# Optimization experiments

Hardware: AMD Instinct MI355X
Metric: run time of the kernel (lower is better)

Reference implementation:

```python
import jax, jax.numpy as jnp
import numpy as np

B, T, N, D, F = 4, 64, 128, 256, 512
LN_EPS = 1e-5


def _ln(x, g, b):
    m = jnp.mean(x, -1, keepdims=True)
    v = jnp.var(x, -1, keepdims=True)
    return (x - m) * jax.lax.rsqrt(v + LN_EPS) * g + b


def _norm_adj(cirmat):
    # dense_to_sparse drops edge weights -> binary adjacency; gcn_norm adds
    # remaining self loops (diag forced to weight 1) and sym-normalizes.
    a = (cirmat != 0).astype(jnp.float32)
    a = jnp.where(jnp.eye(a.shape[0], dtype=bool), 1.0, a)
    deg = a.sum(0)  # aggregation at col index -> in-degree
    dinv = jax.lax.rsqrt(deg)
    return a * dinv[:, None] * dinv[None, :]


def _block_mpnn(x, a_hat, ng, nb, w1, b1, sg, sb, gw, gb, w2, b2):
    # x: [B,T,N,D]. gMLP block whose spatial proj is a GCNConv over the N axis.
    res = x
    h = jax.nn.gelu(_ln(x, ng, nb) @ w1.T + b1, approximate=False)  # [B,T,N,2F]
    u, v = jnp.split(h, 2, axis=-1)
    vn = _ln(v, sg, sb)
    # GCNConv: lin -> normalized aggregation (edge r->c, sum at c) -> +bias
    g = jnp.einsum('rc,btrf->btcf', a_hat, vn @ gw.T) + gb
    return (u * g) @ w2.T + b2 + res


def _block_conv(x, ng, nb, w1, b1, sg, sb, cw, cb, w2, b2):
    # x: [B,N,T,D]. Conv2d(T, T, kernel=(1,3), padding=(0,1)) mixes the T axis
    # as channels with a width-3 window along the feature axis.
    res = x
    h = jax.nn.gelu(_ln(x, ng, nb) @ w1.T + b1, approximate=False)  # [B,N,T,2F]
    u, v = jnp.split(h, 2, axis=-1)
    vn = _ln(v, sg, sb).transpose(0, 2, 1, 3)  # [B,T,N,F] = NCHW
    c = jax.lax.conv_general_dilated(
        vn, cw, window_strides=(1, 1), padding=((0, 0), (1, 1)),
        dimension_numbers=('NCHW', 'OIHW', 'NCHW'))
    g = (c + cb[None, :, None, None]).transpose(0, 2, 1, 3)  # [B,N,T,F]
    return (u * g) @ w2.T + b2 + res


def setup_inputs():
    key = jax.random.key(0)
    cnt = [0]
    def nk():
        cnt[0] += 1
        return jax.random.fold_in(key, cnt[0])
    def rn(shape, s=1.0):
        return jax.random.normal(nk(), shape, jnp.float32) * s
    inp = {}
    inp['x'] = rn((B, T, N, D))
    inp['cirmat'] = jax.random.randint(nk(), (N, N), 0, 2, jnp.int32)
    for p in ('tgu', 'sgu', 'cgu'):
        inp[p + '_ng'] = jnp.ones((D,), jnp.float32)
        inp[p + '_nb'] = jnp.zeros((D,), jnp.float32)
        inp[p + '_w1'] = rn((2 * F, D), 0.02)
        inp[p + '_b1'] = jnp.zeros((2 * F,), jnp.float32)
        inp[p + '_sg'] = jnp.ones((F,), jnp.float32)
        inp[p + '_sb'] = jnp.zeros((F,), jnp.float32)
        inp[p + '_w2'] = rn((D, F), 0.02)
        inp[p + '_b2'] = jnp.zeros((D,), jnp.float32)
    inp['tgu_cw'] = rn((T, T, 1, 3), 0.02)
    inp['tgu_cb'] = jnp.ones((T,), jnp.float32)  # nn.init.constant_(bias, 1.0)
    inp['sgu_gw'] = rn((F, F), 0.02)
    inp['sgu_gb'] = jnp.ones((F,), jnp.float32)
    inp['cgu_gw'] = rn((F, F), 0.02)
    inp['cgu_gb'] = jnp.ones((F,), jnp.float32)
    for n in ('n1', 'n2', 'n3'):
        inp[n + '_g'] = jnp.ones((D,), jnp.float32)
        inp[n + '_b'] = jnp.zeros((D,), jnp.float32)
    inp['w_out'] = rn((D, 3 * D), 0.02)
    inp['b_out'] = jnp.zeros((D,), jnp.float32)
    return inp


def reference(x, cirmat,
              tgu_ng, tgu_nb, tgu_w1, tgu_b1, tgu_sg, tgu_sb, tgu_w2, tgu_b2,
              sgu_ng, sgu_nb, sgu_w1, sgu_b1, sgu_sg, sgu_sb, sgu_w2, sgu_b2,
              cgu_ng, cgu_nb, cgu_w1, cgu_b1, cgu_sg, cgu_sb, cgu_w2, cgu_b2,
              tgu_cw, tgu_cb, sgu_gw, sgu_gb, cgu_gw, cgu_gb,
              n1_g, n1_b, n2_g, n2_b, n3_g, n3_b, w_out, b_out):
    a_hat = _norm_adj(cirmat)
    res = x
    # temporal branch: permute to [B,N,T,D], conv mixer, permute back
    xt = _block_conv(x.transpose(0, 2, 1, 3), tgu_ng, tgu_nb, tgu_w1, tgu_b1,
                     tgu_sg, tgu_sb, tgu_cw, tgu_cb, tgu_w2, tgu_b2)
    xt = _ln(xt.transpose(0, 2, 1, 3), n1_g, n1_b)
    # spatial (GCN) branch; note: the block shadows the passed residual with x
    xs = _ln(_block_mpnn(x, a_hat, sgu_ng, sgu_nb, sgu_w1, sgu_b1, sgu_sg,
                         sgu_sb, sgu_gw, sgu_gb, sgu_w2, sgu_b2), n2_g, n2_b)
    # cycle (GCN) branch (pe=None -> another mpnn block on cirmat_A)
    xc = _ln(_block_mpnn(x, a_hat, cgu_ng, cgu_nb, cgu_w1, cgu_b1, cgu_sg,
                         cgu_sb, cgu_gw, cgu_gb, cgu_w2, cgu_b2), n3_g, n3_b)
    cat = jnp.concatenate([xt, xs, xc], axis=-1)  # [B,T,N,3D]
    # 1x1 Conv2d over the channel (last) dim == linear projection
    return cat @ w_out.T + b_out + res
```

## Files before the change

### kernel.cpp

```cpp
#include <hip/hip_runtime.h>
#include <hip/hip_bf16.h>

typedef unsigned short u16;
typedef unsigned int u32;
typedef __attribute__((ext_vector_type(4))) float f32x4;
typedef __attribute__((ext_vector_type(8))) short short8;

#define DEV __device__ __forceinline__

constexpr int Bc = 4, Tc = 64, Nc = 128, Dc = 256, Fc = 512;
constexpr int R = Bc * Tc * Nc;

constexpr size_t OFF_ABIN = 0;
constexpr size_t OFF_DINV = 65536;
constexpr size_t OFF_COLS = 66560;
constexpr size_t OFF_AHT  = 67584;
constexpr size_t OFF_W1   = 100352;
constexpr size_t OFF_B1   = 1673216;
constexpr size_t OFF_GW   = 1685504;
constexpr size_t OFF_CVEC = 2734080;
constexpr size_t OFF_W2   = 2738176;
constexpr size_t OFF_BW   = 3524608;
constexpr size_t OFF_BTOT = 3917824;
constexpr size_t OFF_CWT  = 3918848;
constexpr size_t OFF_XHAT = 4194304;
constexpr size_t OFF_U    = 20971520;
constexpr size_t OFF_V    = 54525952;
constexpr size_t OFF_S3   = 88080384;
constexpr size_t OFF_Y    = 121634816;
constexpr size_t WS_NEED  = 171966464;

DEV u16 f2b(float f) { __hip_bfloat16 h = __float2bfloat16(f); return *(u16*)&h; }
DEV float b2f(u16 u) { union { u32 i; float f; } v; v.i = ((u32)u) << 16; return v.f; }
DEV u32 pack2(float a, float b) { return (u32)f2b(a) | ((u32)f2b(b) << 16); }
DEV float wave_sum(float s) {
  #pragma unroll
  for (int o = 32; o; o >>= 1) s += __shfl_xor(s, o);
  return s;
}
DEV float gelu(float v) {
  float t = v * v;
  float e = __expf(v * (1.5957691f + 0.0713548162f * t));
  return v - v * __builtin_amdgcn_rcpf(e + 1.0f);
}
DEV void gload16(const u16* g, u16* l) {
  __builtin_amdgcn_global_load_lds((const __attribute__((address_space(1))) void*)g,
                                   (__attribute__((address_space(3))) void*)l, 16, 0, 0);
}
DEV void wait_vm0()   { asm volatile("s_waitcnt vmcnt(0)" ::: "memory");  __builtin_amdgcn_sched_barrier(0); }
DEV void wait_lgkm0() { asm volatile("s_waitcnt lgkmcnt(0)" ::: "memory"); __builtin_amdgcn_sched_barrier(0); }

__global__ void k_adj1(const int* __restrict__ cir, float* __restrict__ aBin) {
  int r = blockIdx.x, c = threadIdx.x;
  aBin[r * 128 + c] = (cir[r * 128 + c] != 0 || r == c) ? 1.f : 0.f;
}
__global__ void k_adj2(const float* __restrict__ aBin, float* __restrict__ dinv) {
  int c = threadIdx.x; float s = 0.f;
  for (int r = 0; r < 128; r++) s += aBin[r * 128 + c];
  dinv[c] = rsqrtf(s);
}
__global__ void k_adj3(const float* __restrict__ aBin, const float* __restrict__ dinv,
                       u16* __restrict__ ahatT) {
  int c = blockIdx.x, r = threadIdx.x;
  ahatT[c * 128 + r] = f2b(aBin[r * 128 + c] * dinv[r] * dinv[c]);
}
__global__ void k_adj4(const float* __restrict__ aBin, const float* __restrict__ dinv,
                       float* __restrict__ colsum) {
  int c = threadIdx.x; float s = 0.f;
  for (int r = 0; r < 128; r++) s += aBin[r * 128 + c] * dinv[r];
  colsum[c] = s * dinv[c];
}

__global__ void k_prep_w1(const float* __restrict__ w1, const float* __restrict__ ng,
                          const float* __restrict__ nb, const float* __restrict__ b1,
                          u16* __restrict__ w1o, float* __restrict__ b1o) {
  int k = blockIdx.x, lane = threadIdx.x;
  float4 wv = *(const float4*)(w1 + k * 256 + lane * 4);
  float4 gv = *(const float4*)(ng + lane * 4);
  float4 bv = *(const float4*)(nb + lane * 4);
  uint2 o; o.x = pack2(wv.x * gv.x, wv.y * gv.y); o.y = pack2(wv.z * gv.z, wv.w * gv.w);
  *(uint2*)(w1o + k * 256 + lane * 4) = o;
  float acc = wv.x * bv.x + wv.y * bv.y + wv.z * bv.z + wv.w * bv.w;
  acc = wave_sum(acc);
  if (lane == 0) b1o[k] = b1[k] + acc;
}
__global__ void k_prep_gw(const float* __restrict__ gw, const float* __restrict__ sg,
                          const float* __restrict__ sb, u16* __restrict__ gwo,
                          float* __restrict__ cvo) {
  int f = blockIdx.x, lane = threadIdx.x;
  float acc = 0.f; uint4 o;
  float4 w0 = *(const float4*)(gw + f * 512 + lane * 8);
  float4 w1 = *(const float4*)(gw + f * 512 + lane * 8 + 4);
  float4 g0 = *(const float4*)(sg + lane * 8);
  float4 g1 = *(const float4*)(sg + lane * 8 + 4);
  float4 b0 = *(const float4*)(sb + lane * 8);
  float4 b1 = *(const float4*)(sb + lane * 8 + 4);
  o.x = pack2(w0.x * g0.x, w0.y * g0.y); o.y = pack2(w0.z * g0.z, w0.w * g0.w);
  o.z = pack2(w1.x * g1.x, w1.y * g1.y); o.w = pack2(w1.z * g1.z, w1.w * g1.w);
  acc = w0.x * b0.x + w0.y * b0.y + w0.z * b0.z + w0.w * b0.w
      + w1.x * b1.x + w1.y * b1.y + w1.z * b1.z + w1.w * b1.w;
  *(uint4*)(gwo + f * 512 + lane * 8) = o;
  acc = wave_sum(acc);
  if (lane == 0) cvo[f] = acc;
}
__global__ void k_b16cvt(const float* __restrict__ src, u16* __restrict__ dst) {
  int idx = (blockIdx.x * 64 + threadIdx.x) * 8;
  float4 a = *(const float4*)(src + idx);
  float4 b = *(const float4*)(src + idx + 4);
  uint4 o; o.x = pack2(a.x, a.y); o.y = pack2(a.z, a.w);
  o.z = pack2(b.x, b.y); o.w = pack2(b.z, b.w);
  *(uint4*)(dst + idx) = o;
}
__global__ void k_prep_wout(const float* __restrict__ wout, const float* __restrict__ bout,
                            const float* __restrict__ g1, const float* __restrict__ b1,
                            const float* __restrict__ g2, const float* __restrict__ b2,
                            const float* __restrict__ g3, const float* __restrict__ b3,
                            u16* __restrict__ bw, float* __restrict__ bt) {
  int o = blockIdx.x, lane = threadIdx.x;
  float acc = 0.f;
  #pragma unroll
  for (int j = 0; j < 12; j++) {
    int c = lane + j * 64;
    int p = c >> 8, i = c & 255;
    const float* gg = (p == 0) ? g1 : (p == 1) ? g2 : g3;
    const float* bb = (p == 0) ? b1 : (p == 1) ? b2 : b3;
    float w = wout[o * 768 + c];
    bw[o * 768 + c] = f2b(w * gg[i]);
    acc += w * bb[i];
  }
  acc = wave_sum(acc);
  if (lane == 0) bt[o] = bout[o] + acc;
}
__global__ void k_prep_cwA(const float* __restrict__ cw, u16* __restrict__ cwA) {
  int t = blockIdx.x, q = threadIdx.x;
  int tap = q >> 6, ti = q & 63;
  cwA[t * 192 + q] = f2b(cw[t * 192 + ti * 3 + tap]);
}

__global__ __launch_bounds__(256) void k_ln1(const float* __restrict__ x, u16* __restrict__ xhat) {
  int row = blockIdx.x * 4 + (threadIdx.x >> 6);
  int lane = threadIdx.x & 63;
  float4 v = *(const float4*)(x + (size_t)row * 256 + lane * 4);
  float s = v.x + v.y + v.z + v.w;
  float s2 = v.x * v.x + v.y * v.y + v.z * v.z + v.w * v.w;
  s = wave_sum(s); s2 = wave_sum(s2);
  float m = s * (1.f / 256.f);
  float var = s2 * (1.f / 256.f) - m * m;
  float rs = rsqrtf(var + 1e-5f);
  uint2 o; o.x = pack2((v.x - m) * rs, (v.y - m) * rs); o.y = pack2((v.z - m) * rs, (v.w - m) * rs);
  *(uint2*)(xhat + (size_t)row * 256 + lane * 4) = o;
}

template <int MODE>
__global__ __launch_bounds__(256) void k_lnv(const u16* __restrict__ Vin, u16* __restrict__ Vout,
                                             const float* __restrict__ sg, const float* __restrict__ sb) {
  int row = blockIdx.x * 4 + (threadIdx.x >> 6);
  int lane = threadIdx.x & 63;
  uint4 raw = *(const uint4*)(Vin + (size_t)row * 512 + lane * 8);
  u16* rp = (u16*)&raw;
  float f[8], s = 0.f, s2 = 0.f;
  #pragma unroll
  for (int j = 0; j < 8; j++) { f[j] = b2f(rp[j]); s += f[j]; s2 += f[j] * f[j]; }
  s = wave_sum(s); s2 = wave_sum(s2);
  float m = s * (1.f / 512.f);
  float var = s2 * (1.f / 512.f) - m * m;
  float rs = rsqrtf(var + 1e-5f);
  float o[8];
  if (MODE == 1) {
    float4 g0 = *(const float4*)(sg + lane * 8);
    float4 g1 = *(const float4*)(sg + lane * 8 + 4);
    float4 b0 = *(const float4*)(sb + lane * 8);
    float4 b1 = *(const float4*)(sb + lane * 8 + 4);
    o[0] = (f[0] - m) * rs * g0.x + b0.x; o[1] = (f[1] - m) * rs * g0.y + b0.y;
    o[2] = (f[2] - m) * rs * g0.z + b0.z; o[3] = (f[3] - m) * rs * g0.w + b0.w;
    o[4] = (f[4] - m) * rs * g1.x + b1.x; o[5] = (f[5] - m) * rs * g1.y + b1.y;
    o[6] = (f[6] - m) * rs * g1.z + b1.z; o[7] = (f[7] - m) * rs * g1.w + b1.w;
  } else {
    #pragma unroll
    for (int j = 0; j < 8; j++) o[j] = (f[j] - m) * rs;
  }
  uint4 ov; ov.x = pack2(o[0], o[1]); ov.y = pack2(o[2], o[3]);
  ov.z = pack2(o[4], o[5]); ov.w = pack2(o[6], o[7]);
  *(uint4*)(Vout + (size_t)row * 512 + lane * 8) = ov;
}

__global__ __launch_bounds__(256) void k_lny(const float* __restrict__ Y, u16* __restrict__ Ycat, int colofs) {
  int row = blockIdx.x * 4 + (threadIdx.x >> 6);
  int lane = threadIdx.x & 63;
  float4 v = *(const float4*)(Y + (size_t)row * 256 + lane * 4);
  float s = v.x + v.y + v.z + v.w;
  float s2 = v.x * v.x + v.y * v.y + v.z * v.z + v.w * v.w;
  s = wave_sum(s); s2 = wave_sum(s2);
  float m = s * (1.f / 256.f);
  float var = s2 * (1.f / 256.f) - m * m;
  float rs = rsqrtf(var + 1e-5f);
  uint2 o; o.x = pack2((v.x - m) * rs, (v.y - m) * rs); o.y = pack2((v.z - m) * rs, (v.w - m) * rs);
  *(uint2*)(Ycat + (size_t)row * 768 + colofs + lane * 4) = o;
}

template <int KDIM>
DEV void stage_tile(const u16* __restrict__ G, u16* lds, int row0, int tid) {
  #pragma unroll
  for (int i = 0; i < 4; i++) {
    int qq = tid + i * 256;
    int row = qq >> 3, kc = qq & 7;
    int kg = kc ^ (row & 7);
    gload16(G + (size_t)(row0 + row) * KDIM + kg * 8, lds + qq * 8);
  }
}

DEV void mfma_step(const u16* As, const u16* Bs, f32x4 (&acc)[4][4], int lane, int wr, int wc) {
  #pragma unroll
  for (int kk = 0; kk < 2; kk++) {
    int kb = kk * 64 + (lane >> 4) * 16;
    short8 af[4], bfr[4];
    #pragma unroll
    for (int m = 0; m < 4; m++) {
      int row = wr * 64 + m * 16 + (lane & 15);
      af[m] = *(const short8*)((const char*)As + ((row * 128 + kb) ^ ((row & 7) << 4)));
    }
    #pragma unroll
    for (int n = 0; n < 4; n++) {
      int col = wc * 64 + n * 16 + (lane & 15);
      bfr[n] = *(const short8*)((const char*)Bs + ((col * 128 + kb) ^ ((col & 7) << 4)));
    }
    #pragma unroll
    for (int m = 0; m < 4; m++)
      #pragma unroll
      for (int n = 0; n < 4; n++)
        acc[m][n] = __builtin_amdgcn_mfma_f32_16x16x32_bf16(af[m], bfr[n], acc[m][n], 0, 0, 0);
  }
}

template <int KDIM, int EPI>
__global__ __launch_bounds__(256) void k_gemm(const u16* __restrict__ A, const u16* __restrict__ Bt,
                                              const float* __restrict__ bias,
                                              const float* __restrict__ xres,
                                              void* __restrict__ out0, void* __restrict__ out1) {
  __shared__ __align__(16) u16 lds[4 * 8192];
  u16* As[2] = { lds, lds + 16384 };
  u16* Bs[2] = { lds + 8192, lds + 24576 };
  const int tid = threadIdx.x;
  const int lane = tid & 63, wid = tid >> 6;
  const int wr = wid >> 1, wc = wid & 1;
  const int rowA0 = blockIdx.x * 128;
  const int colB0 = blockIdx.y * 128;
  constexpr int NT = KDIM / 64;

  f32x4 zero = {0.f, 0.f, 0.f, 0.f};
  f32x4 acc[4][4];
  #pragma unroll
  for (int m = 0; m < 4; m++)
    #pragma unroll
    for (int n = 0; n < 4; n++) acc[m][n] = zero;

  stage_tile<KDIM>(A, As[0], rowA0, tid);
  stage_tile<KDIM>(Bt, Bs[0], colB0, tid);
  wait_vm0();
  __builtin_amdgcn_s_barrier();

  #pragma unroll
  for (int it = 0; it < NT; ++it) {
    const int cur = it & 1;
    if (it + 1 < NT) {
      stage_tile<KDIM>(A + (it + 1) * 64, As[cur ^ 1], rowA0, tid);
      stage_tile<KDIM>(Bt + (it + 1) * 64, Bs[cur ^ 1], colB0, tid);
    }
    mfma_step(As[cur], Bs[cur], acc, lane, wr, wc);
    wait_lgkm0();
    wait_vm0();
    __builtin_amdgcn_s_barrier();
  }

  #pragma unroll
  for (int m = 0; m < 4; m++) {
    #pragma unroll
    for (int n = 0; n < 4; n++) {
      int col = colB0 + wc * 64 + n * 16 + (lane & 15);
      #pragma unroll
      for (int r = 0; r < 4; r++) {
        int row = rowA0 + wr * 64 + m * 16 + (lane >> 4) * 4 + r;
        float v = acc[m][n][r];
        if (EPI == 0) {
          v = gelu(v + bias[col]);
          u16 hv = f2b(v);
          if (col < 512) ((u16*)out0)[(size_t)row * 512 + col] = hv;
          else           ((u16*)out1)[(size_t)row * 512 + col - 512] = hv;
        } else {
          v += bias[col] + xres[(size_t)row * 256 + col];
          ((float*)out0)[(size_t)row * 256 + col] = v;
        }
      }
    }
  }
}

__global__ __launch_bounds__(256) void k_gcn(const u16* __restrict__ A, const u16* __restrict__ Bt,
                                             const u16* __restrict__ U, const u16* __restrict__ ahatT,
                                             const float* __restrict__ colsum, const float* __restrict__ cvec,
                                             const float* __restrict__ gb, u16* __restrict__ ug) {
  __shared__ __align__(16) char smem[65536];
  u16* As[2] = { (u16*)smem, (u16*)(smem + 32768) };
  u16* Bs[2] = { (u16*)(smem + 16384), (u16*)(smem + 49152) };
  u16* glinT = (u16*)smem;
  const int tid = threadIdx.x;
  const int lane = tid & 63, wid = tid >> 6;
  const int wr = wid >> 1, wc = wid & 1;
  const int bt = blockIdx.x;
  const int rowA0 = bt * 128;
  const int colB0 = blockIdx.y * 128;

  f32x4 zero = {0.f, 0.f, 0.f, 0.f};
  f32x4 acc[4][4];
  #pragma unroll
  for (int m = 0; m < 4; m++)
    #pragma unroll
    for (int n = 0; n < 4; n++) acc[m][n] = zero;

  stage_tile<512>(A, As[0], rowA0, tid);
  stage_tile<512>(Bt, Bs[0], colB0, tid);
  wait_vm0();
  __builtin_amdgcn_s_barrier();
  #pragma unroll
  for (int it = 0; it < 8; ++it) {
    const int cur = it & 1;
    if (it + 1 < 8) {
      stage_tile<512>(A + (it + 1) * 64, As[cur ^ 1], rowA0, tid);
      stage_tile<512>(Bt + (it + 1) * 64, Bs[cur ^ 1], colB0, tid);
    }
    mfma_step(As[cur], Bs[cur], acc, lane, wr, wc);
    wait_lgkm0();
    wait_vm0();
    __builtin_amdgcn_s_barrier();
  }

  #pragma unroll
  for (int m = 0; m < 4; m++) {
    #pragma unroll
    for (int n = 0; n < 4; n++) {
      int f = wc * 64 + n * 16 + (lane & 15);
      int n0 = wr * 64 + m * 16 + (lane >> 4) * 4;
      u32* p = (u32*)(glinT + f * 136 + n0);
      p[0] = pack2(acc[m][n][0], acc[m][n][1]);
      p[1] = pack2(acc[m][n][2], acc[m][n][3]);
    }
  }
  __syncthreads();

  f32x4 acc2[4][4];
  #pragma unroll
  for (int m = 0; m < 4; m++)
    #pragma unroll
    for (int n = 0; n < 4; n++) acc2[m][n] = zero;
  #pragma unroll
  for (int ks = 0; ks < 4; ks++) {
    short8 a2[4], b2v[4];
    #pragma unroll
    for (int m = 0; m < 4; m++) {
      int c = wr * 64 + m * 16 + (lane & 15);
      a2[m] = *(const short8*)(ahatT + c * 128 + ks * 32 + (lane >> 4) * 8);
    }
    #pragma unroll
    for (int n = 0; n < 4; n++) {
      int f = wc * 64 + n * 16 + (lane & 15);
      b2v[n] = *(const short8*)(glinT + f * 136 + ks * 32 + (lane >> 4) * 8);
    }
    #pragma unroll
    for (int m = 0; m < 4; m++)
      #pragma unroll
      for (int n = 0; n < 4; n++)
        acc2[m][n] = __builtin_amdgcn_mfma_f32_16x16x32_bf16(a2[m], b2v[n], acc2[m][n], 0, 0, 0);
  }

  #pragma unroll
  for (int m = 0; m < 4; m++) {
    #pragma unroll
    for (int n = 0; n < 4; n++) {
      int fl = wc * 64 + n * 16 + (lane & 15);
      int fg = colB0 + fl;
      float cv = cvec[fg], gbv = gb[fg];
      #pragma unroll
      for (int r = 0; r < 4; r++) {
        int c = wr * 64 + m * 16 + (lane >> 4) * 4 + r;
        size_t row = (size_t)(rowA0 + c) * 512 + fg;
        float g = b2f(U[row]) * (acc2[m][n][r] + colsum[c] * cv + gbv);
        ug[row] = f2b(g);
      }
    }
  }
}

__global__ __launch_bounds__(256) void k_convm(const u16* __restrict__ vn, const u16* __restrict__ U,
                                               const u16* __restrict__ cwA, const float* __restrict__ cb,
                                               u16* __restrict__ ug) {
  __shared__ __align__(16) u16 vnT[258 * 72];
  int bx = blockIdx.x;
  int n = bx & 127, b = (bx >> 7) & 3, h = bx >> 9;
  int tid = threadIdx.x;
  int lane = tid & 63, wid = tid >> 6;

  {
    int ti = tid & 63;
    size_t rowbase = ((size_t)((b * 64 + ti) * 128 + n)) * 512;
    #pragma unroll
    for (int it = 0; it < 8; it++) {
      int fq = (tid >> 6) + it * 4;
      uint4 raw = *(const uint4*)(vn + rowbase + h * 256 + fq * 8);
      u16* rp = (u16*)&raw;
      int vr = fq * 8 + 1;
      #pragma unroll
      for (int j = 0; j < 8; j++) vnT[(vr + j) * 72 + ti] = rp[j];
    }
    if (tid < 64) {
      vnT[0 * 72 + ti]   = (h == 0) ? (u16)0 : vn[rowbase + 255];
      vnT[257 * 72 + ti] = (h == 1) ? (u16)0 : vn[rowbase + 256];
    }
  }
  __syncthreads();

  f32x4 zero = {0.f, 0.f, 0.f, 0.f};
  f32x4 acc[4][4];
  #pragma unroll
  for (int m = 0; m < 4; m++)
    #pragma unroll
    for (int nn = 0; nn < 4; nn++) acc[m][nn] = zero;

  #pragma unroll
  for (int s = 0; s < 6; s++) {
    int tap = s >> 1;
    int K0 = s * 32;
    int tig = (s & 1) * 32 + (lane >> 4) * 8;
    short8 af[4], bf[4];
    #pragma unroll
    for (int m = 0; m < 4; m++) {
      int t = m * 16 + (lane & 15);
      af[m] = *(const short8*)(cwA + t * 192 + K0 + (lane >> 4) * 8);
    }
    #pragma unroll
    for (int nn = 0; nn < 4; nn++) {
      int fl = wid * 64 + nn * 16 + (lane & 15);
      int vr = fl + tap;
      bf[nn] = *(const short8*)(vnT + vr * 72 + tig);
    }
    #pragma unroll
    for (int m = 0; m < 4; m++)
      #pragma unroll
      for (int nn = 0; nn < 4; nn++)
        acc[m][nn] = __builtin_amdgcn_mfma_f32_16x16x32_bf16(af[m], bf[nn], acc[m][nn], 0, 0, 0);
  }

  #pragma unroll
  for (int m = 0; m < 4; m++) {
    #pragma unroll
    for (int nn = 0; nn < 4; nn++) {
      int fl = wid * 64 + nn * 16 + (lane & 15);
      int fg = h * 256 + fl;
      #pragma unroll
      for (int r = 0; r < 4; r++) {
        int t = m * 16 + (lane >> 4) * 4 + r;
        size_t row = ((size_t)((b * 64 + t) * 128 + n)) * 512 + fg;
        float g = b2f(U[row]) * (acc[m][nn][r] + cb[t]);
        ug[row] = f2b(g);
      }
    }
  }
}

extern "C" void kernel_launch(void* const* d_in, const int* in_sizes, int n_in,
                              void* d_out, int out_size, void* d_ws, size_t ws_size,
                              hipStream_t stream) {
  if (ws_size < WS_NEED) return;
  const float* x = (const float*)d_in[0];
  const int* cir = (const int*)d_in[1];
  auto F32 = [&](int i) { return (const float*)d_in[i]; };

  char* W = (char*)d_ws;
  float* aBin   = (float*)(W + OFF_ABIN);
  float* dinv   = (float*)(W + OFF_DINV);
  float* colsum = (float*)(W + OFF_COLS);
  u16*   ahatT  = (u16*)(W + OFF_AHT);
  u16*   W1c    = (u16*)(W + OFF_W1);
  float* b1c    = (float*)(W + OFF_B1);
  u16*   GWc    = (u16*)(W + OFF_GW);
  float* cvec   = (float*)(W + OFF_CVEC);
  u16*   W2c    = (u16*)(W + OFF_W2);
  u16*   BW     = (u16*)(W + OFF_BW);
  float* btot   = (float*)(W + OFF_BTOT);
  u16*   cwA    = (u16*)(W + OFF_CWT);
  u16*   xhat   = (u16*)(W + OFF_XHAT);
  u16*   Ub     = (u16*)(W + OFF_U);
  u16*   Vb     = (u16*)(W + OFF_V);
  u16*   S3     = (u16*)(W + OFF_S3);
  u16*   Ycat   = (u16*)(W + OFF_Y);

  k_adj1<<<128, 128, 0, stream>>>(cir, aBin);
  k_adj2<<<1, 128, 0, stream>>>(aBin, dinv);
  k_adj3<<<128, 128, 0, stream>>>(aBin, dinv, ahatT);
  k_adj4<<<1, 128, 0, stream>>>(aBin, dinv, colsum);
  for (int p = 0; p < 3; p++) {
    int base = 2 + 8 * p;
    k_prep_w1<<<1024, 64, 0, stream>>>(F32(base + 2), F32(base + 0), F32(base + 1), F32(base + 3),
                                       W1c + (size_t)p * 1024 * 256, b1c + p * 1024);
    k_b16cvt<<<256, 64, 0, stream>>>(F32(base + 6), W2c + (size_t)p * 256 * 512);
  }
  k_prep_gw<<<512, 64, 0, stream>>>(F32(28), F32(14), F32(15), GWc, cvec);
  k_prep_gw<<<512, 64, 0, stream>>>(F32(30), F32(22), F32(23), GWc + 512 * 512, cvec + 512);
  k_prep_wout<<<256, 64, 0, stream>>>(F32(38), F32(39), F32(32), F32(33), F32(34), F32(35),
                                      F32(36), F32(37), BW, btot);
  k_prep_cwA<<<64, 192, 0, stream>>>(F32(26), cwA);

  k_ln1<<<8192, 256, 0, stream>>>(x, xhat);

  k_gemm<256, 0><<<dim3(256, 8), 256, 0, stream>>>(xhat, W1c, b1c, nullptr, Ub, Vb);
  k_lnv<1><<<8192, 256, 0, stream>>>(Vb, S3, F32(6), F32(7));
  k_convm<<<1024, 256, 0, stream>>>(S3, Ub, cwA, F32(27), Vb);
  k_gemm<512, 2><<<dim3(256, 2), 256, 0, stream>>>(Vb, W2c, F32(9), x, (void*)S3, nullptr);
  k_lny<<<8192, 256, 0, stream>>>((const float*)S3, Ycat, 0);

  k_gemm<256, 0><<<dim3(256, 8), 256, 0, stream>>>(xhat, W1c + (size_t)1 * 1024 * 256, b1c + 1024,
                                                   nullptr, Ub, Vb);
  k_lnv<0><<<8192, 256, 0, stream>>>(Vb, S3, nullptr, nullptr);
  k_gcn<<<dim3(256, 4), 256, 0, stream>>>(S3, GWc, Ub, ahatT, colsum, cvec, F32(29), Vb);
  k_gemm<512, 2><<<dim3(256, 2), 256, 0, stream>>>(Vb, W2c + (size_t)1 * 256 * 512, F32(17), x,
                                                   (void*)S3, nullptr);
  k_lny<<<8192, 256, 0, stream>>>((const float*)S3, Ycat, 256);

  k_gemm<256, 0><<<dim3(256, 8), 256, 0, stream>>>(xhat, W1c + (size_t)2 * 1024 * 256, b1c + 2048,
                                                   nullptr, Ub, Vb);
  k_lnv<0><<<8192, 256, 0, stream>>>(Vb, S3, nullptr, nullptr);
  k_gcn<<<dim3(256, 4), 256, 0, stream>>>(S3, GWc + 512 * 512, Ub, ahatT, colsum, cvec + 512, F32(31), Vb);
  k_gemm<512, 2><<<dim3(256, 2), 256, 0, stream>>>(Vb, W2c + (size_t)2 * 256 * 512, F32(25), x,
                                                   (void*)S3, nullptr);
  k_lny<<<8192, 256, 0, stream>>>((const float*)S3, Ycat, 512);

  k_gemm<768, 2><<<dim3(256, 2), 256, 0, stream>>>(Ycat, BW, btot, x, d_out, nullptr);
}
```

Before: 595.0 us.

## Fold GCN-branch LayerNorm into GEMM epilogues and deepen k-loop prefetch

The W1 GEMM epilogue now accumulates per-row sum and sum-of-squares of the v half via shuffles and atomics. The GCN kernel then applies the LayerNorm algebraically on its output, using rs*acc - rs*mean*rowsum(gw*sg). This removes the separate k_lnv pass and its full read/write of V for the two GCN branches. The GEMM k-loop also moves to a two-stage prefetch with vmcnt(8) partial waits, and the adjacency precompute skips the intermediate float matrix. In exchange it adds atomics, memsets and a one-pass variance computation that is less numerically robust.

```diff
diff --git a/kernel.cpp b/kernel.cpp
--- a/kernel.cpp
+++ b/kernel.cpp
@@ -11,18 +11,19 @@
 constexpr int Bc = 4, Tc = 64, Nc = 128, Dc = 256, Fc = 512;
 constexpr int R = Bc * Tc * Nc;
 
-constexpr size_t OFF_ABIN = 0;
-constexpr size_t OFF_DINV = 65536;
-constexpr size_t OFF_COLS = 66560;
-constexpr size_t OFF_AHT  = 67584;
-constexpr size_t OFF_W1   = 100352;
-constexpr size_t OFF_B1   = 1673216;
-constexpr size_t OFF_GW   = 1685504;
-constexpr size_t OFF_CVEC = 2734080;
-constexpr size_t OFF_W2   = 2738176;
-constexpr size_t OFF_BW   = 3524608;
-constexpr size_t OFF_BTOT = 3917824;
-constexpr size_t OFF_CWT  = 3918848;
+constexpr size_t OFF_DINV = 0;
+constexpr size_t OFF_COLS = 1024;
+constexpr size_t OFF_AHT  = 2048;
+constexpr size_t OFF_W1   = 34816;
+constexpr size_t OFF_B1   = 1607680;
+constexpr size_t OFF_GW   = 1619968;
+constexpr size_t OFF_CVEC = 2668544;
+constexpr size_t OFF_GWS  = 2672640;
+constexpr size_t OFF_W2   = 2676736;
+constexpr size_t OFF_BW   = 3463168;
+constexpr size_t OFF_BTOT = 3856384;
+constexpr size_t OFF_CWA  = 3857408;
+constexpr size_t OFF_VST  = 3881984;
 constexpr size_t OFF_XHAT = 4194304;
 constexpr size_t OFF_U    = 20971520;
 constexpr size_t OFF_V    = 54525952;
@@ -47,27 +48,27 @@
   __builtin_amdgcn_global_load_lds((const __attribute__((address_space(1))) void*)g,
                                    (__attribute__((address_space(3))) void*)l, 16, 0, 0);
 }
+DEV void wait_lgkm0() { asm volatile("s_waitcnt lgkmcnt(0)" ::: "memory"); __builtin_amdgcn_sched_barrier(0); }
 DEV void wait_vm0()   { asm volatile("s_waitcnt vmcnt(0)" ::: "memory");  __builtin_amdgcn_sched_barrier(0); }
-DEV void wait_lgkm0() { asm volatile("s_waitcnt lgkmcnt(0)" ::: "memory"); __builtin_amdgcn_sched_barrier(0); }
-
-__global__ void k_adj1(const int* __restrict__ cir, float* __restrict__ aBin) {
-  int r = blockIdx.x, c = threadIdx.x;
-  aBin[r * 128 + c] = (cir[r * 128 + c] != 0 || r == c) ? 1.f : 0.f;
-}
-__global__ void k_adj2(const float* __restrict__ aBin, float* __restrict__ dinv) {
+DEV void wait_vm8()   { asm volatile("s_waitcnt vmcnt(8)" ::: "memory");  __builtin_amdgcn_sched_barrier(0); }
+
+DEV float adj(const int* cir, int r, int c) {
+  return (cir[r * 128 + c] != 0 || r == c) ? 1.f : 0.f;
+}
+__global__ void k_adj2(const int* __restrict__ cir, float* __restrict__ dinv) {
   int c = threadIdx.x; float s = 0.f;
-  for (int r = 0; r < 128; r++) s += aBin[r * 128 + c];
+  for (int r = 0; r < 128; r++) s += adj(cir, r, c);
   dinv[c] = rsqrtf(s);
 }
-__global__ void k_adj3(const float* __restrict__ aBin, const float* __restrict__ dinv,
+__global__ void k_adj3(const int* __restrict__ cir, const float* __restrict__ dinv,
                        u16* __restrict__ ahatT) {
   int c = blockIdx.x, r = threadIdx.x;
-  ahatT[c * 128 + r] = f2b(aBin[r * 128 + c] * dinv[r] * dinv[c]);
-}
-__global__ void k_adj4(const float* __restrict__ aBin, const float* __restrict__ dinv,
+  ahatT[c * 128 + r] = f2b(adj(cir, r, c) * dinv[r] * dinv[c]);
+}
+__global__ void k_adj4(const int* __restrict__ cir, const float* __restrict__ dinv,
                        float* __restrict__ colsum) {
   int c = threadIdx.x; float s = 0.f;
-  for (int r = 0; r < 128; r++) s += aBin[r * 128 + c] * dinv[r];
+  for (int r = 0; r < 128; r++) s += adj(cir, r, c) * dinv[r];
   colsum[c] = s * dinv[c];
 }
 
@@ -86,22 +87,25 @@
 }
 __global__ void k_prep_gw(const float* __restrict__ gw, const float* __restrict__ sg,
                           const float* __restrict__ sb, u16* __restrict__ gwo,
-                          float* __restrict__ cvo) {
+                          float* __restrict__ cvo, float* __restrict__ gwso) {
   int f = blockIdx.x, lane = threadIdx.x;
-  float acc = 0.f; uint4 o;
+  uint4 o;
   float4 w0 = *(const float4*)(gw + f * 512 + lane * 8);
   float4 w1 = *(const float4*)(gw + f * 512 + lane * 8 + 4);
   float4 g0 = *(const float4*)(sg + lane * 8);
   float4 g1 = *(const float4*)(sg + lane * 8 + 4);
   float4 b0 = *(const float4*)(sb + lane * 8);
   float4 b1 = *(const float4*)(sb + lane * 8 + 4);
-  o.x = pack2(w0.x * g0.x, w0.y * g0.y); o.y = pack2(w0.z * g0.z, w0.w * g0.w);
-  o.z = pack2(w1.x * g1.x, w1.y * g1.y); o.w = pack2(w1.z * g1.z, w1.w * g1.w);
-  acc = w0.x * b0.x + w0.y * b0.y + w0.z * b0.z + w0.w * b0.w
-      + w1.x * b1.x + w1.y * b1.y + w1.z * b1.z + w1.w * b1.w;
+  float p0 = w0.x * g0.x, p1 = w0.y * g0.y, p2 = w0.z * g0.z, p3 = w0.w * g0.w;
+  float p4 = w1.x * g1.x, p5 = w1.y * g1.y, p6 = w1.z * g1.z, p7 = w1.w * g1.w;
+  o.x = pack2(p0, p1); o.y = pack2(p2, p3); o.z = pack2(p4, p5); o.w = pack2(p6, p7);
   *(uint4*)(gwo + f * 512 + lane * 8) = o;
-  acc = wave_sum(acc);
-  if (lane == 0) cvo[f] = acc;
+  float accb = w0.x * b0.x + w0.y * b0.y + w0.z * b0.z + w0.w * b0.w
+             + w1.x * b1.x + w1.y * b1.y + w1.z * b1.z + w1.w * b1.w;
+  float accg = p0 + p1 + p2 + p3 + p4 + p5 + p6 + p7;
+  accb = wave_sum(accb);
+  accg = wave_sum(accg);
+  if (lane == 0) { cvo[f] = accb; gwso[f] = accg; }
 }
 __global__ void k_b16cvt(const float* __restrict__ src, u16* __restrict__ dst) {
   int idx = (blockIdx.x * 64 + threadIdx.x) * 8;
@@ -151,7 +155,6 @@
   *(uint2*)(xhat + (size_t)row * 256 + lane * 4) = o;
 }
 
-template <int MODE>
 __global__ __launch_bounds__(256) void k_lnv(const u16* __restrict__ Vin, u16* __restrict__ Vout,
                                              const float* __restrict__ sg, const float* __restrict__ sb) {
   int row = blockIdx.x * 4 + (threadIdx.x >> 6);
@@ -165,20 +168,15 @@
   float m = s * (1.f / 512.f);
   float var = s2 * (1.f / 512.f) - m * m;
   float rs = rsqrtf(var + 1e-5f);
+  float4 g0 = *(const float4*)(sg + lane * 8);
+  float4 g1 = *(const float4*)(sg + lane * 8 + 4);
+  float4 b0 = *(const float4*)(sb + lane * 8);
+  float4 b1 = *(const float4*)(sb + lane * 8 + 4);
   float o[8];
-  if (MODE == 1) {
-    float4 g0 = *(const float4*)(sg + lane * 8);
-    float4 g1 = *(const float4*)(sg + lane * 8 + 4);
-    float4 b0 = *(const float4*)(sb + lane * 8);
-    float4 b1 = *(const float4*)(sb + lane * 8 + 4);
-    o[0] = (f[0] - m) * rs * g0.x + b0.x; o[1] = (f[1] - m) * rs * g0.y + b0.y;
-    o[2] = (f[2] - m) * rs * g0.z + b0.z; o[3] = (f[3] - m) * rs * g0.w + b0.w;
-    o[4] = (f[4] - m) * rs * g1.x + b1.x; o[5] = (f[5] - m) * rs * g1.y + b1.y;
-    o[6] = (f[6] - m) * rs * g1.z + b1.z; o[7] = (f[7] - m) * rs * g1.w + b1.w;
-  } else {
-    #pragma unroll
-    for (int j = 0; j < 8; j++) o[j] = (f[j] - m) * rs;
-  }
+  o[0] = (f[0] - m) * rs * g0.x + b0.x; o[1] = (f[1] - m) * rs * g0.y + b0.y;
+  o[2] = (f[2] - m) * rs * g0.z + b0.z; o[3] = (f[3] - m) * rs * g0.w + b0.w;
+  o[4] = (f[4] - m) * rs * g1.x + b1.x; o[5] = (f[5] - m) * rs * g1.y + b1.y;
+  o[6] = (f[6] - m) * rs * g1.z + b1.z; o[7] = (f[7] - m) * rs * g1.w + b1.w;
   uint4 ov; ov.x = pack2(o[0], o[1]); ov.y = pack2(o[2], o[3]);
   ov.z = pack2(o[4], o[5]); ov.w = pack2(o[6], o[7]);
   *(uint4*)(Vout + (size_t)row * 512 + lane * 8) = ov;
@@ -232,14 +230,32 @@
   }
 }
 
+template <int KDIM, int NT>
+DEV void pipe_kloop(const u16* __restrict__ A, const u16* __restrict__ Bt, u16* lds,
+                    f32x4 (&acc)[4][4], int rowA0, int colB0, int tid, int lane, int wr, int wc) {
+  #pragma unroll
+  for (int it = 0; it < NT; ++it) {
+    if (it + 1 < NT) wait_vm8();
+    else             wait_vm0();
+    __builtin_amdgcn_s_barrier();
+    const u16* Asc = lds + (it & 1) * 16384;
+    mfma_step(Asc, Asc + 8192, acc, lane, wr, wc);
+    wait_lgkm0();
+    __builtin_amdgcn_s_barrier();
+    if (it + 2 < NT) {
+      stage_tile<KDIM>(A + (it + 2) * 64, lds + (it & 1) * 16384, rowA0, tid);
+      stage_tile<KDIM>(Bt + (it + 2) * 64, lds + (it & 1) * 16384 + 8192, colB0, tid);
+    }
+  }
+}
+
 template <int KDIM, int EPI>
 __global__ __launch_bounds__(256) void k_gemm(const u16* __restrict__ A, const u16* __restrict__ Bt,
                                               const float* __restrict__ bias,
                                               const float* __restrict__ xres,
-                                              void* __restrict__ out0, void* __restrict__ out1) {
-  __shared__ __align__(16) u16 lds[4 * 8192];
-  u16* As[2] = { lds, lds + 16384 };
-  u16* Bs[2] = { lds + 8192, lds + 24576 };
+                                              void* __restrict__ out0, void* __restrict__ out1,
+                                              float* __restrict__ vstat) {
+  __shared__ __align__(16) u16 lds[4 * 16384 / 2];
   const int tid = threadIdx.x;
   const int lane = tid & 63, wid = tid >> 6;
   const int wr = wid >> 1, wc = wid & 1;
@@ -254,40 +270,63 @@
     #pragma unroll
     for (int n = 0; n < 4; n++) acc[m][n] = zero;
 
-  stage_tile<KDIM>(A, As[0], rowA0, tid);
-  stage_tile<KDIM>(Bt, Bs[0], colB0, tid);
-  wait_vm0();
-  __builtin_amdgcn_s_barrier();
-
-  #pragma unroll
-  for (int it = 0; it < NT; ++it) {
-    const int cur = it & 1;
-    if (it + 1 < NT) {
-      stage_tile<KDIM>(A + (it + 1) * 64, As[cur ^ 1], rowA0, tid);
-      stage_tile<KDIM>(Bt + (it + 1) * 64, Bs[cur ^ 1], colB0, tid);
-    }
-    mfma_step(As[cur], Bs[cur], acc, lane, wr, wc);
-    wait_lgkm0();
-    wait_vm0();
-    __builtin_amdgcn_s_barrier();
-  }
-
-  #pragma unroll
-  for (int m = 0; m < 4; m++) {
-    #pragma unroll
-    for (int n = 0; n < 4; n++) {
-      int col = colB0 + wc * 64 + n * 16 + (lane & 15);
-      #pragma unroll
-      for (int r = 0; r < 4; r++) {
-        int row = rowA0 + wr * 64 + m * 16 + (lane >> 4) * 4 + r;
-        float v = acc[m][n][r];
-        if (EPI == 0) {
-          v = gelu(v + bias[col]);
+  stage_tile<KDIM>(A, lds, rowA0, tid);
+  stage_tile<KDIM>(Bt, lds + 8192, colB0, tid);
+  stage_tile<KDIM>(A + 64, lds + 16384, rowA0, tid);
+  stage_tile<KDIM>(Bt + 64, lds + 24576, colB0, tid);
+  pipe_kloop<KDIM, NT>(A, Bt, lds, acc, rowA0, colB0, tid, lane, wr, wc);
+
+  if (EPI == 0) {
+    float s1a[4][4], s2a[4][4];
+    #pragma unroll
+    for (int m = 0; m < 4; m++)
+      #pragma unroll
+      for (int r = 0; r < 4; r++) { s1a[m][r] = 0.f; s2a[m][r] = 0.f; }
+    #pragma unroll
+    for (int m = 0; m < 4; m++) {
+      #pragma unroll
+      for (int n = 0; n < 4; n++) {
+        int col = colB0 + wc * 64 + n * 16 + (lane & 15);
+        float bcol = bias[col];
+        #pragma unroll
+        for (int r = 0; r < 4; r++) {
+          int row = rowA0 + wr * 64 + m * 16 + (lane >> 4) * 4 + r;
+          float v = gelu(acc[m][n][r] + bcol);
+          s1a[m][r] += v; s2a[m][r] += v * v;
           u16 hv = f2b(v);
           if (col < 512) ((u16*)out0)[(size_t)row * 512 + col] = hv;
           else           ((u16*)out1)[(size_t)row * 512 + col - 512] = hv;
-        } else {
-          v += bias[col] + xres[(size_t)row * 256 + col];
+        }
+      }
+    }
+    if (vstat != nullptr && colB0 >= 512) {
+      #pragma unroll
+      for (int m = 0; m < 4; m++) {
+        #pragma unroll
+        for (int r = 0; r < 4; r++) {
+          float s1 = s1a[m][r], s2 = s2a[m][r];
+          s1 += __shfl_xor(s1, 1); s2 += __shfl_xor(s2, 1);
+          s1 += __shfl_xor(s1, 2); s2 += __shfl_xor(s2, 2);
+          s1 += __shfl_xor(s1, 4); s2 += __shfl_xor(s2, 4);
+          s1 += __shfl_xor(s1, 8); s2 += __shfl_xor(s2, 8);
+          if ((lane & 15) == 0) {
+            int row = rowA0 + wr * 64 + m * 16 + (lane >> 4) * 4 + r;
+            atomicAdd(vstat + 2 * row, s1);
+            atomicAdd(vstat + 2 * row + 1, s2);
+          }
+        }
+      }
+    }
+  } else {
+    #pragma unroll
+    for (int m = 0; m < 4; m++) {
+      #pragma unroll
+      for (int n = 0; n < 4; n++) {
+        int col = colB0 + wc * 64 + n * 16 + (lane & 15);
+        #pragma unroll
+        for (int r = 0; r < 4; r++) {
+          int row = rowA0 + wr * 64 + m * 16 + (lane >> 4) * 4 + r;
+          float v = acc[m][n][r] + bias[col] + xres[(size_t)row * 256 + col];
           ((float*)out0)[(size_t)row * 256 + col] = v;
         }
       }
@@ -298,16 +337,15 @@
 __global__ __launch_bounds__(256) void k_gcn(const u16* __restrict__ A, const u16* __restrict__ Bt,
                                              const u16* __restrict__ U, const u16* __restrict__ ahatT,
                                              const float* __restrict__ colsum, const float* __restrict__ cvec,
-                                             const float* __restrict__ gb, u16* __restrict__ ug) {
+                                             const float* __restrict__ gwsum, const float* __restrict__ gb,
+                                             const float* __restrict__ vstat, u16* __restrict__ ug) {
   __shared__ __align__(16) char smem[65536];
-  u16* As[2] = { (u16*)smem, (u16*)(smem + 32768) };
-  u16* Bs[2] = { (u16*)(smem + 16384), (u16*)(smem + 49152) };
+  u16* lds = (u16*)smem;
   u16* glinT = (u16*)smem;
   const int tid = threadIdx.x;
   const int lane = tid & 63, wid = tid >> 6;
   const int wr = wid >> 1, wc = wid & 1;
-  const int bt = blockIdx.x;
-  const int rowA0 = bt * 128;
+  const int rowA0 = blockIdx.x * 128;
   const int colB0 = blockIdx.y * 128;
 
   f32x4 zero = {0.f, 0.f, 0.f, 0.f};
@@ -317,32 +355,39 @@
     #pragma unroll
     for (int n = 0; n < 4; n++) acc[m][n] = zero;
 
-  stage_tile<512>(A, As[0], rowA0, tid);
-  stage_tile<512>(Bt, Bs[0], colB0, tid);
-  wait_vm0();
-  __builtin_amdgcn_s_barrier();
-  #pragma unroll
-  for (int it = 0; it < 8; ++it) {
-    const int cur = it & 1;
-    if (it + 1 < 8) {
-      stage_tile<512>(A + (it + 1) * 64, As[cur ^ 1], rowA0, tid);
-      stage_tile<512>(Bt + (it + 1) * 64, Bs[cur ^ 1], colB0, tid);
-    }
-    mfma_step(As[cur], Bs[cur], acc, lane, wr, wc);
-    wait_lgkm0();
-    wait_vm0();
-    __builtin_amdgcn_s_barrier();
-  }
+  stage_tile<512>(A, lds, rowA0, tid);
+  stage_tile<512>(Bt, lds + 8192, colB0, tid);
+  stage_tile<512>(A + 64, lds + 16384, rowA0, tid);
+  stage_tile<512>(Bt + 64, lds + 24576, colB0, tid);
+  pipe_kloop<512, 8>(A, Bt, lds, acc, rowA0, colB0, tid, lane, wr, wc);
+
+  float rsv[4][4], rsmv[4][4];
+  #pragma unroll
+  for (int m = 0; m < 4; m++)
+    #pragma unroll
+    for (int r = 0; r < 4; r++) {
+      int row = rowA0 + wr * 64 + m * 16 + (lane >> 4) * 4 + r;
+      float st0 = vstat[2 * row], st1 = vstat[2 * row + 1];
+      float mean = st0 * (1.f / 512.f);
+      float var = fmaxf(st1 * (1.f / 512.f) - mean * mean, 0.f);
+      float rs = rsqrtf(var + 1e-5f);
+      rsv[m][r] = rs; rsmv[m][r] = rs * mean;
+    }
 
   #pragma unroll
   for (int m = 0; m < 4; m++) {
     #pragma unroll
     for (int n = 0; n < 4; n++) {
-      int f = wc * 64 + n * 16 + (lane & 15);
+      int fl = wc * 64 + n * 16 + (lane & 15);
+      float S = gwsum[colB0 + fl];
       int n0 = wr * 64 + m * 16 + (lane >> 4) * 4;
-      u32* p = (u32*)(glinT + f * 136 + n0);
-      p[0] = pack2(acc[m][n][0], acc[m][n][1]);
-      p[1] = pack2(acc[m][n][2], acc[m][n][3]);
+      float v0 = rsv[m][0] * acc[m][n][0] - rsmv[m][0] * S;
+      float v1 = rsv[m][1] * acc[m][n][1] - rsmv[m][1] * S;
+      float v2 = rsv[m][2] * acc[m][n][2] - rsmv[m][2] * S;
+      float v3 = rsv[m][3] * acc[m][n][3] - rsmv[m][3] * S;
+      u32* p = (u32*)(glinT + fl * 136 + n0);
+      p[0] = pack2(v0, v1);
+      p[1] = pack2(v2, v3);
     }
   }
   __syncthreads();
@@ -475,7 +520,6 @@
   auto F32 = [&](int i) { return (const float*)d_in[i]; };
 
   char* W = (char*)d_ws;
-  float* aBin   = (float*)(W + OFF_ABIN);
   float* dinv   = (float*)(W + OFF_DINV);
   float* colsum = (float*)(W + OFF_COLS);
   u16*   ahatT  = (u16*)(W + OFF_AHT);
@@ -483,55 +527,57 @@
   float* b1c    = (float*)(W + OFF_B1);
   u16*   GWc    = (u16*)(W + OFF_GW);
   float* cvec   = (float*)(W + OFF_CVEC);
+  float* gws    = (float*)(W + OFF_GWS);
   u16*   W2c    = (u16*)(W + OFF_W2);
   u16*   BW     = (u16*)(W + OFF_BW);
   float* btot   = (float*)(W + OFF_BTOT);
-  u16*   cwA    = (u16*)(W + OFF_CWT);
+  u16*   cwA    = (u16*)(W + OFF_CWA);
+  float* vstat  = (float*)(W + OFF_VST);
   u16*   xhat   = (u16*)(W + OFF_XHAT);
   u16*   Ub     = (u16*)(W + OFF_U);
   u16*   Vb     = (u16*)(W + OFF_V);
   u16*   S3     = (u16*)(W + OFF_S3);
   u16*   Ycat   = (u16*)(W + OFF_Y);
 
-  k_adj1<<<128, 128, 0, stream>>>(cir, aBin);
-  k_adj2<<<1, 128, 0, stream>>>(aBin, dinv);
-  k_adj3<<<128, 128, 0, stream>>>(aBin, dinv, ahatT);
-  k_adj4<<<1, 128, 0, stream>>>(aBin, dinv, colsum);
+  k_adj2<<<1, 128, 0, stream>>>(cir, dinv);
+  k_adj3<<<128, 128, 0, stream>>>(cir, dinv, ahatT);
+  k_adj4<<<1, 128, 0, stream>>>(cir, dinv, colsum);
   for (int p = 0; p < 3; p++) {
     int base = 2 + 8 * p;
     k_prep_w1<<<1024, 64, 0, stream>>>(F32(base + 2), F32(base + 0), F32(base + 1), F32(base + 3),
                                        W1c + (size_t)p * 1024 * 256, b1c + p * 1024);
     k_b16cvt<<<256, 64, 0, stream>>>(F32(base + 6), W2c + (size_t)p * 256 * 512);
   }
-  k_prep_gw<<<512, 64, 0, stream>>>(F32(28), F32(14), F32(15), GWc, cvec);
-  k_prep_gw<<<512, 64, 0, stream>>>(F32(30), F32(22), F32(23), GWc + 512 * 512, cvec + 512);
+  k_prep_gw<<<512, 64, 0, stream>>>(F32(28), F32(14), F32(15), GWc, cvec, gws);
+  k_prep_gw<<<512, 64, 0, stream>>>(F32(30), F32(22), F32(23), GWc + 512 * 512, cvec + 512, gws + 512);
   k_prep_wout<<<256, 64, 0, stream>>>(F32(38), F32(39), F32(32), F32(33), F32(34), F32(35),
                                       F32(36), F32(37), BW, btot);
   k_prep_cwA<<<64, 192, 0, stream>>>(F32(26), cwA);
 
   k_ln1<<<8192, 256, 0, stream>>>(x, xhat);
 
-  k_gemm<256, 0><<<dim3(256, 8), 256, 0, stream>>>(xhat, W1c, b1c, nullptr, Ub, Vb);
-  k_lnv<1><<<8192, 256, 0, stream>>>(Vb, S3, F32(6), F32(7));
+  k_gemm<256, 0><<<dim3(256, 8), 256, 0, stream>>>(xhat, W1c, b1c, nullptr, Ub, Vb, nullptr);
+  k_lnv<<<8192, 256, 0, stream>>>(Vb, S3, F32(6), F32(7));
   k_convm<<<1024, 256, 0, stream>>>(S3, Ub, cwA, F32(27), Vb);
-  k_gemm<512, 2><<<dim3(256, 2), 256, 0, stream>>>(Vb, W2c, F32(9), x, (void*)S3, nullptr);
+  k_gemm<512, 2><<<dim3(256, 2), 256, 0, stream>>>(Vb, W2c, F32(9), x, (void*)S3, nullptr, nullptr);
   k_lny<<<8192, 256, 0, stream>>>((const float*)S3, Ycat, 0);
 
+  hipMemsetAsync(vstat, 0, 262144, stream);
   k_gemm<256, 0><<<dim3(256, 8), 256, 0, stream>>>(xhat, W1c + (size_t)1 * 1024 * 256, b1c + 1024,
-                                                   nullptr, Ub, Vb);
-  k_lnv<0><<<8192, 256, 0, stream>>>(Vb, S3, nullptr, nullptr);
-  k_gcn<<<dim3(256, 4), 256, 0, stream>>>(S3, GWc, Ub, ahatT, colsum, cvec, F32(29), Vb);
-  k_gemm<512, 2><<<dim3(256, 2), 256, 0, stream>>>(Vb, W2c + (size_t)1 * 256 * 512, F32(17), x,
-                                                   (void*)S3, nullptr);
-  k_lny<<<8192, 256, 0, stream>>>((const float*)S3, Ycat, 256);
-
+                                                   nullptr, Ub, Vb, vstat);
+  k_gcn<<<dim3(256, 4), 256, 0, stream>>>(Vb, GWc, Ub, ahatT, colsum, cvec, gws, F32(29), vstat, S3);
+  k_gemm<512, 2><<<dim3(256, 2), 256, 0, stream>>>(S3, W2c + (size_t)1 * 256 * 512, F32(17), x,
+                                                   (void*)Vb, nullptr, nullptr);
+  k_lny<<<8192, 256, 0, stream>>>((const float*)Vb, Ycat, 256);
+
+  hipMemsetAsync(vstat, 0, 262144, stream);
   k_gemm<256, 0><<<dim3(256, 8), 256, 0, stream>>>(xhat, W1c + (size_t)2 * 1024 * 256, b1c + 2048,
-                                                   nullptr, Ub, Vb);
-  k_lnv<0><<<8192, 256, 0, stream>>>(Vb, S3, nullptr, nullptr);
-  k_gcn<<<dim3(256, 4), 256, 0, stream>>>(S3, GWc + 512 * 512, Ub, ahatT, colsum, cvec + 512, F32(31), Vb);
-  k_gemm<512, 2><<<dim3(256, 2), 256, 0, stream>>>(Vb, W2c + (size_t)2 * 256 * 512, F32(25), x,
-                                                   (void*)S3, nullptr);
-  k_lny<<<8192, 256, 0, stream>>>((const float*)S3, Ycat, 512);
-
-  k_gemm<768, 2><<<dim3(256, 2), 256, 0, stream>>>(Ycat, BW, btot, x, d_out, nullptr);
-}
+                                                   nullptr, Ub, Vb, vstat);
+  k_gcn<<<dim3(256, 4), 256, 0, stream>>>(Vb, GWc + 512 * 512, Ub, ahatT, colsum, cvec + 512,
+                                          gws + 512, F32(31), vstat, S3);
+  k_gemm<512, 2><<<dim3(256, 2), 256, 0, stream>>>(S3, W2c + (size_t)2 * 256 * 512, F32(25), x,
+                                                   (void*)Vb, nullptr, nullptr);
+  k_lny<<<8192, 256, 0, stream>>>((const float*)Vb, Ycat, 512);
+
+  k_gemm<768, 2><<<dim3(256, 2), 256, 0, stream>>>(Ycat, BW, btot, x, d_out, nullptr, nullptr);
+}
```

Measured after the change: 578.3 us. 1.03x faster.
